# Performance work log

Measured on AMD Instinct MI355X. Metric: run time of the kernel, lower is better.

Reference implementation:

```python
import jax, jax.numpy as jnp
import numpy as np

BL = 5           # block_len
BS = BL * BL     # block_size = 25
NH = 8           # num_heads
MASK_ONES = 12   # first 12 window positions unmasked (causal raster mask)


def _rel_pos_index():
    coords = np.stack(np.meshgrid(np.arange(BL), np.arange(BL), indexing='ij')).reshape(2, -1)
    rel = coords[:, :, None] - coords[:, None, :]          # [2, 25, 25]
    idx = (rel[0] + BL - 1) * (2 * BL - 1) + (rel[1] + BL - 1)
    return idx                                              # [25, 25] int

_REL_IDX = _rel_pos_index()


def _layernorm(x, w, b, eps=1e-5):
    m = jnp.mean(x, axis=-1, keepdims=True)
    v = jnp.var(x, axis=-1, keepdims=True)
    return (x - m) * jax.lax.rsqrt(v + eps) * w + b


def setup_inputs() -> dict:
    key = jax.random.key(0)
    ks = jax.random.split(key, 16)
    B, C, H, W = 4, 64, 64, 64
    out_dim = 64
    hidden = int(C * 4.0)
    s = lambda k, shape, scale=0.02: jax.random.normal(k, shape, dtype=jnp.float32) * scale
    return {
        'x': jax.random.normal(ks[0], (B, C, H, W), dtype=jnp.float32),
        'norm1_w': jnp.ones((C,), jnp.float32), 'norm1_b': jnp.zeros((C,), jnp.float32),
        'qkv_w': s(ks[1], (3 * C, C)), 'qkv_b': s(ks[2], (3 * C,)),
        'rpb_table': s(ks[3], ((2 * BL - 1) * (2 * BL - 1), NH)),
        'norm2_w': jnp.ones((C,), jnp.float32), 'norm2_b': jnp.zeros((C,), jnp.float32),
        'fc1_w': s(ks[4], (hidden, C)), 'fc1_b': s(ks[5], (hidden,)),
        'fc2_w': s(ks[6], (C, hidden)), 'fc2_b': s(ks[7], (C,)),
        'proj_w': s(ks[8], (out_dim, C)), 'proj_b': s(ks[9], (out_dim,)),
    }


def reference(x, norm1_w, norm1_b, qkv_w, qkv_b, rpb_table,
              norm2_w, norm2_b, fc1_w, fc1_b, fc2_w, fc2_b, proj_w, proj_b):
    B, C, H, W = x.shape
    hd = C // NH
    scale = hd ** (-0.5)

    # F.unfold(kernel=5, pad=2): per-pixel 5x5 neighborhood, channel-major then (kh,kw)
    xp = jnp.pad(x, ((0, 0), (0, 0), (2, 2), (2, 2)))
    patches = jnp.stack([xp[:, :, i:i + H, j:j + W] for i in range(BL) for j in range(BL)], axis=2)  # [B,C,25,H,W]
    x_unfold = patches.reshape(B, C, BS, H * W).transpose(0, 3, 2, 1)  # [B,HW,25,C]

    mask = (jnp.arange(BS) < MASK_ONES).astype(x.dtype)[None, None, :, None]
    x_masked = x_unfold * mask

    out = _layernorm(x_masked, norm1_w, norm1_b)
    qkv = out @ qkv_w.T + qkv_b                                 # [B,HW,25,3C]
    qkv = qkv.reshape(B, H * W, BS, 3, NH, hd).transpose(3, 0, 1, 4, 2, 5)  # [3,B,HW,nh,25,hd]
    q, k, v = qkv[0] * scale, qkv[1], qkv[2]

    attn = jnp.einsum('bpnqd,bpnkd->bpnqk', q, k)               # [B,HW,nh,25,25]
    bias = rpb_table[_REL_IDX.reshape(-1)].reshape(BS, BS, NH).transpose(2, 0, 1)  # [nh,25,25]
    attn = jax.nn.softmax(attn + bias[None, None], axis=-1)

    o = jnp.einsum('bpnqk,bpnkd->bpnqd', attn, v)               # [B,HW,nh,25,hd]
    o = o.transpose(0, 1, 3, 2, 4).reshape(B, H * W, BS, C)
    o = o + x_masked
    out_sumed = jnp.sum(o, axis=2)                              # [B,HW,C]

    y = _layernorm(out_sumed, norm2_w, norm2_b)
    y = jax.nn.gelu(y @ fc1_w.T + fc1_b, approximate=False) @ fc2_w.T + fc2_b
    y = y + out_sumed
    y = y @ proj_w.T + proj_b                                   # [B,HW,out_dim]
    return y.reshape(B, H, W, -1).transpose(0, 3, 1, 2)
```

## Files before the change

### kernel.cpp

```cpp
#include <hip/hip_runtime.h>
#include <hip/hip_bf16.h>


typedef _Float16 h2f __attribute__((ext_vector_type(2)));
typedef _Float16 h8  __attribute__((ext_vector_type(8)));
union u8h { h8 v; h2f p[4]; };
union pk4 { _Float16 h[4]; unsigned int u[2]; };

__device__ __forceinline__ float fdot2f(h2f a, h2f b, float c) {
#if defined(__has_builtin)
#if __has_builtin(__builtin_amdgcn_fdot2)
    return __builtin_amdgcn_fdot2(a, b, c, false);
#else
    return c + (float)a.x*(float)b.x + (float)a.y*(float)b.y;
#endif
#else
    return c + (float)a.x*(float)b.x + (float)a.y*(float)b.y;
#endif
}
__device__ __forceinline__ float dot8(u8h a, u8h b) {
    float c = 0.f;
    c = fdot2f(a.p[0], b.p[0], c);
    c = fdot2f(a.p[1], b.p[1], c);
    c = fdot2f(a.p[2], b.p[2], c);
    c = fdot2f(a.p[3], b.p[3], c);
    return c;
}
__device__ __forceinline__ float frcp(float x) {
#if defined(__has_builtin)
#if __has_builtin(__builtin_amdgcn_rcpf)
    return __builtin_amdgcn_rcpf(x);
#else
    return 1.0f/x;
#endif
#else
    return 1.0f/x;
#endif
}
__device__ __forceinline__ u8h ldh8(const _Float16* p) { u8h r; __builtin_memcpy(&r, p, 16); return r; }
__device__ __forceinline__ void st16(_Float16* d, const float4& v) { __builtin_memcpy(d, &v, 16); }
__device__ __forceinline__ float4 ld16(const _Float16* p) { float4 v; __builtin_memcpy(&v, p, 16); return v; }

#define SC 0.35355339059327373f

__global__ __launch_bounds__(1024) void k_qkv(
    const float* __restrict__ x, const float* __restrict__ n1w, const float* __restrict__ n1b,
    const float* __restrict__ qw, const float* __restrict__ qb, const float* __restrict__ rpb,
    const float* __restrict__ w1, const float* __restrict__ w2, const float* __restrict__ pw,
    _Float16* __restrict__ qkvh, _Float16* __restrict__ qkvc_h, _Float16* __restrict__ eb7,
    _Float16* __restrict__ w1h, _Float16* __restrict__ w2h, _Float16* __restrict__ pwh,
    float* __restrict__ osT)
{
    __shared__ float smem[6208];
    const int t = threadIdx.x, bid = blockIdx.x;
    if (bid < 256) {
        _Float16* sOut = (_Float16*)smem;
        const int pix = t & 63, g = t >> 6;
        const int p = bid*64 + pix;
        const int b = p >> 12, hw = p & 4095;
        const float* xp = x + (size_t)b*262144 + hw;
        float xr[64]; float s = 0.f, s2 = 0.f;
        #pragma unroll
        for (int c = 0; c < 64; ++c) { float v = xp[(size_t)c*4096]; xr[c] = v; s += v; s2 += v*v; }
        float m = s*0.015625f;
        float rstd = rsqrtf(fmaxf(s2*0.015625f - m*m, 0.f) + 1e-5f);
        #pragma unroll
        for (int c = 0; c < 64; ++c) xr[c] = (xr[c] - m)*rstd*n1w[c] + n1b[c];
        #pragma unroll
        for (int i4 = 0; i4 < 12; i4 += 4) {
            const int o = g*12 + i4;
            const float* wr = qw + o*64;
            float a0 = qb[o], a1 = qb[o+1], a2 = qb[o+2], a3 = qb[o+3];
            #pragma unroll 16
            for (int c = 0; c < 64; ++c) {
                float xv = xr[c];
                a0 += xv*wr[c]; a1 += xv*wr[64+c]; a2 += xv*wr[128+c]; a3 += xv*wr[192+c];
            }
            pk4 pk;
            pk.h[0]=(_Float16)a0; pk.h[1]=(_Float16)a1; pk.h[2]=(_Float16)a2; pk.h[3]=(_Float16)a3;
            __builtin_memcpy(sOut + pix*194 + o, &pk, 8);
        }
        __syncthreads();
        for (int i = t; i < 1536; i += 1024) {
            int pp = i/24, d4 = i%24;
            ((float4*)qkvh)[(size_t)bid*1536 + i] = ld16(sOut + pp*194 + d4*8);
        }
        return;
    }
    if (bid < 512) {
        float* sxp = smem;
        const int plane = bid - 256;
        for (int i = t; i < 4624; i += 1024) sxp[i] = 0.f;
        __syncthreads();
        const float* xp = x + (size_t)plane*4096;
        for (int i = t; i < 4096; i += 1024) {
            int r = i >> 6, w = i & 63;
            sxp[(r + 2)*68 + (w + 2)] = xp[i];
        }
        __syncthreads();
        const int c = plane & 63, b = plane >> 6;
        float* op = osT + (size_t)c*16384 + b*4096;
        for (int i = t; i < 4096; i += 1024) {
            int r = i >> 6, w = i & 63;
            const float* s0 = sxp + r*68 + w;
            float sv = s0[0]+s0[1]+s0[2]+s0[3]+s0[4]
                     + s0[68]+s0[69]+s0[70]+s0[71]+s0[72]
                     + s0[136]+s0[137];
            op[i] = sv;
        }
        return;
    }
    if (bid < 520) {
        const int cid = bid - 512;
        for (int i = t; i < 4608; i += 1024) {
            int j = cid*4608 + i;
            if (j < 16384)      w1h[j]          = (_Float16)w1[j];
            else if (j < 32768) w2h[j - 16384]  = (_Float16)w2[j - 16384];
            else                pwh[j - 32768]  = (_Float16)pw[j - 32768];
        }
        return;
    }
    if (t < 192) {
        float acc = qb[t];
        for (int c = 0; c < 64; ++c) acc += n1b[c]*qw[t*64 + c];
        qkvc_h[t] = (_Float16)acc;
    }
    for (int i = t; i < 3200; i += 1024) {
        int j = i & 7, hf = (i >> 3) & 1, r = i >> 4;
        int h = r/25, q = r - h*25;
        float v = 0.f;
        if (j < 6) {
            int k = hf*6 + j;
            int ridx = (q/5 - k/5 + 4)*9 + (q%5 - k%5 + 4);
            v = __expf(rpb[ridx*8 + h]);
        } else if (j == 6 && hf) {
            for (int k = 12; k < 25; ++k) {
                int ridx = (q/5 - k/5 + 4)*9 + (q%5 - k%5 + 4);
                v += __expf(rpb[ridx*8 + h]);
            }
        }
        eb7[i] = (_Float16)v;
    }
}

__global__ __launch_bounds__(512) void k_attn(
    const _Float16* __restrict__ qkvh, const _Float16* __restrict__ qkvc_h,
    const _Float16* __restrict__ eb7g, float* __restrict__ osT)
{
    __shared__ _Float16 sq[108*194];
    __shared__ alignas(16) _Float16 seb[3200];
    __shared__ alignas(16) _Float16 sqc[192];
    const int t = threadIdx.x;
    const int p0 = blockIdx.x*32;
    const int b = p0 >> 12, hw0 = p0 & 4095, hrow = hw0 >> 6, w0c = hw0 & 63;

    for (int i = t; i < 1600; i += 512) ((unsigned int*)seb)[i] = ((const unsigned int*)eb7g)[i];
    if (t < 96) ((unsigned int*)sqc)[t] = ((const unsigned int*)qkvc_h)[t];
    for (int i = t; i < 2592; i += 512) {
        int row = i/24, d4 = i%24;
        int rr = row/36, cc = row%36;
        int gr = hrow - 2 + rr, gc = w0c - 2 + cc;
        float4 v = (gr >= 0 && gc >= 0 && gc < 64)
            ? ((const float4*)qkvh)[(size_t)((b << 12) + (gr << 6) + gc)*24 + d4]
            : ((const float4*)qkvc_h)[d4];
        st16(sq + row*194 + d4*8, v);
    }
    __syncthreads();

    const int pix = t & 31, hf = (t >> 5) & 1, h = t >> 6, hb = h*8;
    int rws[6];
    #pragma unroll
    for (int j = 0; j < 6; ++j) { int k = hf*6 + j; rws[j] = (k/5)*36 + pix + (k%5); }
    u8h kreg[7];
    #pragma unroll
    for (int j = 0; j < 6; ++j) kreg[j] = ldh8(sq + rws[j]*194 + 64 + hb);
    kreg[6] = hf ? ldh8(sqc + 64 + hb) : kreg[0];
    u8h qcu = ldh8(sqc + hb);
    float edc[7];
    #pragma unroll
    for (int j = 0; j < 7; ++j) edc[j] = __expf(dot8(qcu, kreg[j])*SC);
    float w[7];
    #pragma unroll
    for (int j = 0; j < 7; ++j) w[j] = 0.f;
    const _Float16* ebbase = seb + h*400 + hf*8;

    for (int sIdx = 0; sIdx < 12; ++sIdx) {
        int rq = (sIdx/5)*36 + pix + (sIdx%5);
        u8h qu = ldh8(sq + rq*194 + hb);
        h8 eb8; __builtin_memcpy(&eb8, ebbase + sIdx*16, 16);
        float e[7]; float rs = 0.f;
        #pragma unroll
        for (int j = 0; j < 7; ++j) {
            float ev = __expf(dot8(qu, kreg[j])*SC)*(float)eb8[j];
            e[j] = ev; rs += ev;
        }
        rs += __shfl_xor(rs, 32);
        float inv = frcp(rs);
        #pragma unroll
        for (int j = 0; j < 7; ++j) w[j] += e[j]*inv;
    }
    for (int q = 12; q < 25; ++q) {
        h8 eb8; __builtin_memcpy(&eb8, ebbase + q*16, 16);
        float e[7]; float rs = 0.f;
        #pragma unroll
        for (int j = 0; j < 7; ++j) {
            float ev = edc[j]*(float)eb8[j];
            e[j] = ev; rs += ev;
        }
        rs += __shfl_xor(rs, 32);
        float inv = frcp(rs);
        #pragma unroll
        for (int j = 0; j < 7; ++j) w[j] += e[j]*inv;
    }
    float out[8];
    #pragma unroll
    for (int d = 0; d < 8; ++d) out[d] = 0.f;
    #pragma unroll
    for (int j = 0; j < 7; ++j) {
        const _Float16* vp = (j < 6) ? (sq + rws[j]*194 + 128 + hb)
                                     : (hf ? sqc + 128 + hb : sq + rws[0]*194 + 128 + hb);
        u8h vv = ldh8(vp);
        float wj = w[j];
        #pragma unroll
        for (int d4 = 0; d4 < 4; ++d4) {
            h2f pr = vv.p[d4];
            out[d4*2]   += wj*(float)pr.x;
            out[d4*2+1] += wj*(float)pr.y;
        }
    }
    #pragma unroll
    for (int d = 0; d < 8; ++d) out[d] += __shfl_xor(out[d], 32);
    const int p = p0 + pix, dbase = hf*4;
    float* op = osT + (size_t)(hb + dbase)*16384 + p;
    op[0]     += out[dbase];
    op[16384] += out[dbase + 1];
    op[32768] += out[dbase + 2];
    op[49152] += out[dbase + 3];
}

__global__ __launch_bounds__(512) void k_mlp(
    const float* __restrict__ osT, const float* __restrict__ n2w, const float* __restrict__ n2b,
    const float* __restrict__ b1, const float* __restrict__ b2, const float* __restrict__ pb,
    const _Float16* __restrict__ w1h, const _Float16* __restrict__ w2h, const _Float16* __restrict__ pwh,
    float* __restrict__ out)
{
    __shared__ float sRed[2][576];
    __shared__ h2f  sAv[64*33];
    __shared__ alignas(16) _Float16 sH[64*258];
    __shared__ alignas(16) _Float16 sY[64*74];
    const int t = threadIdx.x;
    const int pix = t & 63, g = t >> 6;
    const int p = blockIdx.x*64 + pix;
    const int c0 = g*8;
    float v[8]; float ps = 0.f, ps2 = 0.f;
    #pragma unroll
    for (int j = 0; j < 8; ++j) {
        float vv = osT[(size_t)(c0 + j)*16384 + p];
        v[j] = vv; ps += vv; ps2 += vv*vv;
    }
    sRed[0][pix*9 + g] = ps;
    sRed[1][pix*9 + g] = ps2;
    __syncthreads();
    float s = 0.f, s2 = 0.f;
    #pragma unroll
    for (int gg = 0; gg < 8; ++gg) { s += sRed[0][pix*9 + gg]; s2 += sRed[1][pix*9 + gg]; }
    float m = s*0.015625f;
    float rstd = rsqrtf(fmaxf(s2*0.015625f - m*m, 0.f) + 1e-5f);
    #pragma unroll
    for (int k = 0; k < 4; ++k) {
        float e0 = (v[2*k]   - m)*rstd*n2w[c0 + 2*k]   + n2b[c0 + 2*k];
        float e1 = (v[2*k+1] - m)*rstd*n2w[c0 + 2*k+1] + n2b[c0 + 2*k+1];
        sAv[pix*33 + g*4 + k] = h2f{(_Float16)e0, (_Float16)e1};
    }
    __syncthreads();
    const h2f* avr = sAv + pix*33;
    #pragma unroll
    for (int i4 = 0; i4 < 32; i4 += 4) {
        const int j = g*32 + i4;
        const h2f* wr = (const h2f*)(w1h + (size_t)j*64);
        float a0 = b1[j], a1 = b1[j+1], a2 = b1[j+2], a3 = b1[j+3];
        #pragma unroll
        for (int cp = 0; cp < 32; ++cp) {
            h2f xv = avr[cp];
            a0 = fdot2f(xv, wr[cp],      a0);
            a1 = fdot2f(xv, wr[32 + cp], a1);
            a2 = fdot2f(xv, wr[64 + cp], a2);
            a3 = fdot2f(xv, wr[96 + cp], a3);
        }
        sH[pix*258 + j]     = (_Float16)(0.5f*a0*(1.f + erff(a0*0.70710678f)));
        sH[pix*258 + j + 1] = (_Float16)(0.5f*a1*(1.f + erff(a1*0.70710678f)));
        sH[pix*258 + j + 2] = (_Float16)(0.5f*a2*(1.f + erff(a2*0.70710678f)));
        sH[pix*258 + j + 3] = (_Float16)(0.5f*a3*(1.f + erff(a3*0.70710678f)));
    }
    __syncthreads();
    const h2f* hr = (const h2f*)(sH + pix*258);
    #pragma unroll
    for (int m4 = 0; m4 < 8; m4 += 4) {
        const int o = g*8 + m4;
        const h2f* wr = (const h2f*)(w2h + (size_t)o*256);
        float a0 = b2[o], a1 = b2[o+1], a2 = b2[o+2], a3 = b2[o+3];
        #pragma unroll 32
        for (int jp = 0; jp < 128; ++jp) {
            h2f hv = hr[jp];
            a0 = fdot2f(hv, wr[jp],       a0);
            a1 = fdot2f(hv, wr[128 + jp], a1);
            a2 = fdot2f(hv, wr[256 + jp], a2);
            a3 = fdot2f(hv, wr[384 + jp], a3);
        }
        a0 += osT[(size_t)o*16384 + p];
        a1 += osT[(size_t)(o+1)*16384 + p];
        a2 += osT[(size_t)(o+2)*16384 + p];
        a3 += osT[(size_t)(o+3)*16384 + p];
        sY[pix*74 + o]     = (_Float16)a0;
        sY[pix*74 + o + 1] = (_Float16)a1;
        sY[pix*74 + o + 2] = (_Float16)a2;
        sY[pix*74 + o + 3] = (_Float16)a3;
    }
    __syncthreads();
    const h2f* yr = (const h2f*)(sY + pix*74);
    const int bimg = p >> 12, hw = p & 4095, hh = hw >> 6;
    #pragma unroll
    for (int m4 = 0; m4 < 8; m4 += 4) {
        const int o = g*8 + m4;
        const h2f* wr = (const h2f*)(pwh + (size_t)o*64);
        float a0 = pb[o], a1 = pb[o+1], a2 = pb[o+2], a3 = pb[o+3];
        #pragma unroll
        for (int cp = 0; cp < 32; ++cp) {
            h2f yv = yr[cp];
            a0 = fdot2f(yv, wr[cp],      a0);
            a1 = fdot2f(yv, wr[32 + cp], a1);
            a2 = fdot2f(yv, wr[64 + cp], a2);
            a3 = fdot2f(yv, wr[96 + cp], a3);
        }
        float* ob = out + ((size_t)((bimg*64 + o)*64 + hh))*64 + pix;
        ob[0]     = a0;
        ob[4096]  = a1;
        ob[8192]  = a2;
        ob[12288] = a3;
    }
}

extern "C" void kernel_launch(void* const* d_in, const int* in_sizes, int n_in,
                              void* d_out, int out_size, void* d_ws, size_t ws_size,
                              hipStream_t stream) {
    const float* x   = (const float*)d_in[0];
    const float* n1w = (const float*)d_in[1];
    const float* n1b = (const float*)d_in[2];
    const float* qw  = (const float*)d_in[3];
    const float* qb  = (const float*)d_in[4];
    const float* rpb = (const float*)d_in[5];
    const float* n2w = (const float*)d_in[6];
    const float* n2b = (const float*)d_in[7];
    const float* w1  = (const float*)d_in[8];
    const float* b1  = (const float*)d_in[9];
    const float* w2  = (const float*)d_in[10];
    const float* b2  = (const float*)d_in[11];
    const float* pw  = (const float*)d_in[12];
    const float* pb  = (const float*)d_in[13];
    float* out = (float*)d_out;

    float* ws = (float*)d_ws;
    _Float16* qkvh   = (_Float16*)ws;
    float*    osT    = ws + 1572864;
    _Float16* qkvc_h = (_Float16*)(ws + 2621440);
    _Float16* eb7    = (_Float16*)(ws + 2621536);
    _Float16* w1h    = (_Float16*)(ws + 2623136);
    _Float16* w2h    = (_Float16*)(ws + 2631328);
    _Float16* pwh    = (_Float16*)(ws + 2639520);

    hipLaunchKernelGGL(k_qkv, dim3(521), dim3(1024), 0, stream,
                       x, n1w, n1b, qw, qb, rpb, w1, w2, pw,
                       qkvh, qkvc_h, eb7, w1h, w2h, pwh, osT);
    hipLaunchKernelGGL(k_attn, dim3(512), dim3(512), 0, stream,
                       qkvh, qkvc_h, eb7, osT);
    hipLaunchKernelGGL(k_mlp, dim3(256), dim3(512), 0, stream,
                       osT, n2w, n2b, b1, b2, pb, w1h, w2h, pwh, out);
}
```

Baseline: 217.8 us.

## Fuse attention and MLP kernels; stage x through shared memory in QKV

Merges the attention kernel and the MLP/projection kernel into one launch. Each 32-pixel block keeps its attention output plus residual in shared memory and runs layernorm, fc1, GELU, fc2 and proj from there, so the osT read-modify-write and the second global read of osT go away. Shared memory regions are aliased across phases. The QKV kernel now loads its x tile cooperatively into padded shared memory before the per-pixel layernorm. The trade-offs are extra barriers, larger shared memory per block (possibly lower occupancy) and smaller MLP blocks that reload weights more often.

```diff
diff --git a/kernel.cpp b/kernel.cpp
--- a/kernel.cpp
+++ b/kernel.cpp
@@ -51,17 +51,22 @@
     _Float16* __restrict__ w1h, _Float16* __restrict__ w2h, _Float16* __restrict__ pwh,
     float* __restrict__ osT)
 {
-    __shared__ float smem[6208];
+    __shared__ float smem[10368];
     const int t = threadIdx.x, bid = blockIdx.x;
     if (bid < 256) {
-        _Float16* sOut = (_Float16*)smem;
+        float* sXf = smem;
+        _Float16* sOut = (_Float16*)(smem + 4160);
+        const int p0 = bid*64;
+        const int b = p0 >> 12, hw0 = p0 & 4095;
+        for (int i = t; i < 4096; i += 1024) {
+            int c = i >> 6, pp = i & 63;
+            sXf[pp*65 + c] = x[(size_t)b*262144 + (size_t)c*4096 + hw0 + pp];
+        }
+        __syncthreads();
         const int pix = t & 63, g = t >> 6;
-        const int p = bid*64 + pix;
-        const int b = p >> 12, hw = p & 4095;
-        const float* xp = x + (size_t)b*262144 + hw;
         float xr[64]; float s = 0.f, s2 = 0.f;
         #pragma unroll
-        for (int c = 0; c < 64; ++c) { float v = xp[(size_t)c*4096]; xr[c] = v; s += v; s2 += v*v; }
+        for (int c = 0; c < 64; ++c) { float v = sXf[pix*65 + c]; xr[c] = v; s += v; s2 += v*v; }
         float m = s*0.015625f;
         float rstd = rsqrtf(fmaxf(s2*0.015625f - m*m, 0.f) + 1e-5f);
         #pragma unroll
@@ -143,13 +148,25 @@
     }
 }
 
-__global__ __launch_bounds__(512) void k_attn(
+__global__ __launch_bounds__(512) void k_fused(
     const _Float16* __restrict__ qkvh, const _Float16* __restrict__ qkvc_h,
-    const _Float16* __restrict__ eb7g, float* __restrict__ osT)
+    const _Float16* __restrict__ eb7g, const float* __restrict__ osT,
+    const float* __restrict__ n2w, const float* __restrict__ n2b,
+    const float* __restrict__ b1, const float* __restrict__ b2, const float* __restrict__ pb,
+    const _Float16* __restrict__ w1h, const _Float16* __restrict__ w2h, const _Float16* __restrict__ pwh,
+    float* __restrict__ out)
 {
-    __shared__ _Float16 sq[108*194];
-    __shared__ alignas(16) _Float16 seb[3200];
-    __shared__ alignas(16) _Float16 sqc[192];
+    __shared__ alignas(16) char smem[57040];
+    _Float16* sq   = (_Float16*)(smem);
+    _Float16* seb  = (_Float16*)(smem + 41920);
+    _Float16* sqc  = (_Float16*)(smem + 48320);
+    float*    sOs  = (float*)   (smem + 48704);
+    _Float16* sH   = (_Float16*)(smem);
+    h2f*      sAv  = (h2f*)     (smem + 16512);
+    float*    sRW  = (float*)   (smem + 20880);
+    float*    sMR  = (float*)   (smem + 23008);
+    _Float16* sY   = (_Float16*)(smem + 41920);
+
     const int t = threadIdx.x;
     const int p0 = blockIdx.x*32;
     const int b = p0 >> 12, hw0 = p0 & 4095, hrow = hw0 >> 6, w0c = hw0 & 63;
@@ -165,139 +182,147 @@
             : ((const float4*)qkvc_h)[d4];
         st16(sq + row*194 + d4*8, v);
     }
-    __syncthreads();
-
-    const int pix = t & 31, hf = (t >> 5) & 1, h = t >> 6, hb = h*8;
-    int rws[6];
+    for (int i = t; i < 2048; i += 512) {
+        int c = i >> 5, pp = i & 31;
+        sOs[pp*65 + c] = osT[(size_t)c*16384 + p0 + pp];
+    }
+    __syncthreads();
+
+    {
+        const int pix = t & 31, hf = (t >> 5) & 1, h = t >> 6, hb = h*8;
+        int rws[6];
+        #pragma unroll
+        for (int j = 0; j < 6; ++j) { int k = hf*6 + j; rws[j] = (k/5)*36 + pix + (k%5); }
+        u8h kreg[7];
+        #pragma unroll
+        for (int j = 0; j < 6; ++j) kreg[j] = ldh8(sq + rws[j]*194 + 64 + hb);
+        kreg[6] = hf ? ldh8(sqc + 64 + hb) : kreg[0];
+        u8h qcu = ldh8(sqc + hb);
+        float edc[7];
+        #pragma unroll
+        for (int j = 0; j < 7; ++j) edc[j] = __expf(dot8(qcu, kreg[j])*SC);
+        float w[7];
+        #pragma unroll
+        for (int j = 0; j < 7; ++j) w[j] = 0.f;
+        const _Float16* ebbase = seb + h*400 + hf*8;
+
+        for (int sIdx = 0; sIdx < 12; ++sIdx) {
+            int rq = (sIdx/5)*36 + pix + (sIdx%5);
+            u8h qu = ldh8(sq + rq*194 + hb);
+            h8 eb8; __builtin_memcpy(&eb8, ebbase + sIdx*16, 16);
+            float e[7]; float rs = 0.f;
+            #pragma unroll
+            for (int j = 0; j < 7; ++j) {
+                float ev = __expf(dot8(qu, kreg[j])*SC)*(float)eb8[j];
+                e[j] = ev; rs += ev;
+            }
+            rs += __shfl_xor(rs, 32);
+            float inv = frcp(rs);
+            #pragma unroll
+            for (int j = 0; j < 7; ++j) w[j] += e[j]*inv;
+        }
+        for (int q = 12; q < 25; ++q) {
+            h8 eb8; __builtin_memcpy(&eb8, ebbase + q*16, 16);
+            float e[7]; float rs = 0.f;
+            #pragma unroll
+            for (int j = 0; j < 7; ++j) {
+                float ev = edc[j]*(float)eb8[j];
+                e[j] = ev; rs += ev;
+            }
+            rs += __shfl_xor(rs, 32);
+            float inv = frcp(rs);
+            #pragma unroll
+            for (int j = 0; j < 7; ++j) w[j] += e[j]*inv;
+        }
+        float o8[8];
+        #pragma unroll
+        for (int d = 0; d < 8; ++d) o8[d] = 0.f;
+        #pragma unroll
+        for (int j = 0; j < 7; ++j) {
+            const _Float16* vp = (j < 6) ? (sq + rws[j]*194 + 128 + hb)
+                                         : (hf ? sqc + 128 + hb : sq + rws[0]*194 + 128 + hb);
+            u8h vv = ldh8(vp);
+            float wj = w[j];
+            #pragma unroll
+            for (int d4 = 0; d4 < 4; ++d4) {
+                h2f pr = vv.p[d4];
+                o8[d4*2]   += wj*(float)pr.x;
+                o8[d4*2+1] += wj*(float)pr.y;
+            }
+        }
+        #pragma unroll
+        for (int d = 0; d < 8; ++d) o8[d] += __shfl_xor(o8[d], 32);
+        const int c0 = hb + hf*4;
+        float* ap = sOs + pix*65 + c0;
+        #pragma unroll
+        for (int j = 0; j < 4; ++j) ap[j] += o8[hf*4 + j];
+    }
+    __syncthreads();
+
+    const int pix = t & 31, sl = t >> 5;
+    const int c4 = sl*4;
+    float ps = 0.f, ps2 = 0.f;
+    float vch[4];
     #pragma unroll
-    for (int j = 0; j < 6; ++j) { int k = hf*6 + j; rws[j] = (k/5)*36 + pix + (k%5); }
-    u8h kreg[7];
-    #pragma unroll
-    for (int j = 0; j < 6; ++j) kreg[j] = ldh8(sq + rws[j]*194 + 64 + hb);
-    kreg[6] = hf ? ldh8(sqc + 64 + hb) : kreg[0];
-    u8h qcu = ldh8(sqc + hb);
-    float edc[7];
-    #pragma unroll
-    for (int j = 0; j < 7; ++j) edc[j] = __expf(dot8(qcu, kreg[j])*SC);
-    float w[7];
-    #pragma unroll
-    for (int j = 0; j < 7; ++j) w[j] = 0.f;
-    const _Float16* ebbase = seb + h*400 + hf*8;
-
-    for (int sIdx = 0; sIdx < 12; ++sIdx) {
-        int rq = (sIdx/5)*36 + pix + (sIdx%5);
-        u8h qu = ldh8(sq + rq*194 + hb);
-        h8 eb8; __builtin_memcpy(&eb8, ebbase + sIdx*16, 16);
-        float e[7]; float rs = 0.f;
-        #pragma unroll
-        for (int j = 0; j < 7; ++j) {
-            float ev = __expf(dot8(qu, kreg[j])*SC)*(float)eb8[j];
-            e[j] = ev; rs += ev;
-        }
-        rs += __shfl_xor(rs, 32);
-        float inv = frcp(rs);
-        #pragma unroll
-        for (int j = 0; j < 7; ++j) w[j] += e[j]*inv;
-    }
-    for (int q = 12; q < 25; ++q) {
-        h8 eb8; __builtin_memcpy(&eb8, ebbase + q*16, 16);
-        float e[7]; float rs = 0.f;
-        #pragma unroll
-        for (int j = 0; j < 7; ++j) {
-            float ev = edc[j]*(float)eb8[j];
-            e[j] = ev; rs += ev;
-        }
-        rs += __shfl_xor(rs, 32);
-        float inv = frcp(rs);
-        #pragma unroll
-        for (int j = 0; j < 7; ++j) w[j] += e[j]*inv;
-    }
-    float out[8];
-    #pragma unroll
-    for (int d = 0; d < 8; ++d) out[d] = 0.f;
-    #pragma unroll
-    for (int j = 0; j < 7; ++j) {
-        const _Float16* vp = (j < 6) ? (sq + rws[j]*194 + 128 + hb)
-                                     : (hf ? sqc + 128 + hb : sq + rws[0]*194 + 128 + hb);
-        u8h vv = ldh8(vp);
-        float wj = w[j];
-        #pragma unroll
-        for (int d4 = 0; d4 < 4; ++d4) {
-            h2f pr = vv.p[d4];
-            out[d4*2]   += wj*(float)pr.x;
-            out[d4*2+1] += wj*(float)pr.y;
-        }
-    }
-    #pragma unroll
-    for (int d = 0; d < 8; ++d) out[d] += __shfl_xor(out[d], 32);
-    const int p = p0 + pix, dbase = hf*4;
-    float* op = osT + (size_t)(hb + dbase)*16384 + p;
-    op[0]     += out[dbase];
-    op[16384] += out[dbase + 1];
-    op[32768] += out[dbase + 2];
-    op[49152] += out[dbase + 3];
-}
-
-__global__ __launch_bounds__(512) void k_mlp(
-    const float* __restrict__ osT, const float* __restrict__ n2w, const float* __restrict__ n2b,
-    const float* __restrict__ b1, const float* __restrict__ b2, const float* __restrict__ pb,
-    const _Float16* __restrict__ w1h, const _Float16* __restrict__ w2h, const _Float16* __restrict__ pwh,
-    float* __restrict__ out)
-{
-    __shared__ float sRed[2][576];
-    __shared__ h2f  sAv[64*33];
-    __shared__ alignas(16) _Float16 sH[64*258];
-    __shared__ alignas(16) _Float16 sY[64*74];
-    const int t = threadIdx.x;
-    const int pix = t & 63, g = t >> 6;
-    const int p = blockIdx.x*64 + pix;
-    const int c0 = g*8;
-    float v[8]; float ps = 0.f, ps2 = 0.f;
-    #pragma unroll
-    for (int j = 0; j < 8; ++j) {
-        float vv = osT[(size_t)(c0 + j)*16384 + p];
-        v[j] = vv; ps += vv; ps2 += vv*vv;
-    }
-    sRed[0][pix*9 + g] = ps;
-    sRed[1][pix*9 + g] = ps2;
-    __syncthreads();
-    float s = 0.f, s2 = 0.f;
-    #pragma unroll
-    for (int gg = 0; gg < 8; ++gg) { s += sRed[0][pix*9 + gg]; s2 += sRed[1][pix*9 + gg]; }
-    float m = s*0.015625f;
-    float rstd = rsqrtf(fmaxf(s2*0.015625f - m*m, 0.f) + 1e-5f);
-    #pragma unroll
-    for (int k = 0; k < 4; ++k) {
-        float e0 = (v[2*k]   - m)*rstd*n2w[c0 + 2*k]   + n2b[c0 + 2*k];
-        float e1 = (v[2*k+1] - m)*rstd*n2w[c0 + 2*k+1] + n2b[c0 + 2*k+1];
-        sAv[pix*33 + g*4 + k] = h2f{(_Float16)e0, (_Float16)e1};
-    }
-    __syncthreads();
-    const h2f* avr = sAv + pix*33;
-    #pragma unroll
-    for (int i4 = 0; i4 < 32; i4 += 4) {
-        const int j = g*32 + i4;
-        const h2f* wr = (const h2f*)(w1h + (size_t)j*64);
-        float a0 = b1[j], a1 = b1[j+1], a2 = b1[j+2], a3 = b1[j+3];
-        #pragma unroll
-        for (int cp = 0; cp < 32; ++cp) {
-            h2f xv = avr[cp];
-            a0 = fdot2f(xv, wr[cp],      a0);
-            a1 = fdot2f(xv, wr[32 + cp], a1);
-            a2 = fdot2f(xv, wr[64 + cp], a2);
-            a3 = fdot2f(xv, wr[96 + cp], a3);
-        }
-        sH[pix*258 + j]     = (_Float16)(0.5f*a0*(1.f + erff(a0*0.70710678f)));
-        sH[pix*258 + j + 1] = (_Float16)(0.5f*a1*(1.f + erff(a1*0.70710678f)));
-        sH[pix*258 + j + 2] = (_Float16)(0.5f*a2*(1.f + erff(a2*0.70710678f)));
-        sH[pix*258 + j + 3] = (_Float16)(0.5f*a3*(1.f + erff(a3*0.70710678f)));
-    }
-    __syncthreads();
-    const h2f* hr = (const h2f*)(sH + pix*258);
-    #pragma unroll
-    for (int m4 = 0; m4 < 8; m4 += 4) {
-        const int o = g*8 + m4;
+    for (int j = 0; j < 4; ++j) {
+        float v = sOs[pix*65 + c4 + j];
+        vch[j] = v; ps += v; ps2 += v*v;
+    }
+    ps  += __shfl_xor(ps, 32);
+    ps2 += __shfl_xor(ps2, 32);
+    const int wv = t >> 6;
+    if (((t >> 5) & 1) == 0) {
+        sRW[(wv*33 + pix)*2]     = ps;
+        sRW[(wv*33 + pix)*2 + 1] = ps2;
+    }
+    __syncthreads();
+    if (t < 32) {
+        float s = 0.f, s2 = 0.f;
+        #pragma unroll
+        for (int g = 0; g < 8; ++g) { s += sRW[(g*33 + t)*2]; s2 += sRW[(g*33 + t)*2 + 1]; }
+        float m = s*0.015625f;
+        sMR[t*2]     = m;
+        sMR[t*2 + 1] = rsqrtf(fmaxf(s2*0.015625f - m*m, 0.f) + 1e-5f);
+    }
+    __syncthreads();
+    {
+        float m = sMR[pix*2], r = sMR[pix*2 + 1];
+        #pragma unroll
+        for (int j = 0; j < 2; ++j) {
+            float e0 = (vch[2*j]   - m)*r*n2w[c4 + 2*j]   + n2b[c4 + 2*j];
+            float e1 = (vch[2*j+1] - m)*r*n2w[c4 + 2*j+1] + n2b[c4 + 2*j+1];
+            sAv[pix*34 + sl*2 + j] = h2f{(_Float16)e0, (_Float16)e1};
+        }
+    }
+    __syncthreads();
+
+    {
+        const h2f* avr = sAv + pix*34;
+        #pragma unroll
+        for (int i4 = 0; i4 < 16; i4 += 4) {
+            const int j = sl*16 + i4;
+            const h2f* wr = (const h2f*)(w1h + (size_t)j*64);
+            float a0 = b1[j], a1 = b1[j+1], a2 = b1[j+2], a3 = b1[j+3];
+            #pragma unroll
+            for (int cp = 0; cp < 32; ++cp) {
+                h2f xv = avr[cp];
+                a0 = fdot2f(xv, wr[cp],      a0);
+                a1 = fdot2f(xv, wr[32 + cp], a1);
+                a2 = fdot2f(xv, wr[64 + cp], a2);
+                a3 = fdot2f(xv, wr[96 + cp], a3);
+            }
+            sH[pix*258 + j]     = (_Float16)(0.5f*a0*(1.f + erff(a0*0.70710678f)));
+            sH[pix*258 + j + 1] = (_Float16)(0.5f*a1*(1.f + erff(a1*0.70710678f)));
+            sH[pix*258 + j + 2] = (_Float16)(0.5f*a2*(1.f + erff(a2*0.70710678f)));
+            sH[pix*258 + j + 3] = (_Float16)(0.5f*a3*(1.f + erff(a3*0.70710678f)));
+        }
+    }
+    __syncthreads();
+
+    {
+        const int o = sl*4;
         const h2f* wr = (const h2f*)(w2h + (size_t)o*256);
+        const h2f* hr = (const h2f*)(sH + pix*258);
         float a0 = b2[o], a1 = b2[o+1], a2 = b2[o+2], a3 = b2[o+3];
         #pragma unroll 32
         for (int jp = 0; jp < 128; ++jp) {
@@ -307,22 +332,21 @@
             a2 = fdot2f(hv, wr[256 + jp], a2);
             a3 = fdot2f(hv, wr[384 + jp], a3);
         }
-        a0 += osT[(size_t)o*16384 + p];
-        a1 += osT[(size_t)(o+1)*16384 + p];
-        a2 += osT[(size_t)(o+2)*16384 + p];
-        a3 += osT[(size_t)(o+3)*16384 + p];
+        a0 += sOs[pix*65 + o];
+        a1 += sOs[pix*65 + o + 1];
+        a2 += sOs[pix*65 + o + 2];
+        a3 += sOs[pix*65 + o + 3];
         sY[pix*74 + o]     = (_Float16)a0;
         sY[pix*74 + o + 1] = (_Float16)a1;
         sY[pix*74 + o + 2] = (_Float16)a2;
         sY[pix*74 + o + 3] = (_Float16)a3;
     }
     __syncthreads();
-    const h2f* yr = (const h2f*)(sY + pix*74);
-    const int bimg = p >> 12, hw = p & 4095, hh = hw >> 6;
-    #pragma unroll
-    for (int m4 = 0; m4 < 8; m4 += 4) {
-        const int o = g*8 + m4;
+
+    {
+        const int o = sl*4;
         const h2f* wr = (const h2f*)(pwh + (size_t)o*64);
+        const h2f* yr = (const h2f*)(sY + pix*74);
         float a0 = pb[o], a1 = pb[o+1], a2 = pb[o+2], a3 = pb[o+3];
         #pragma unroll
         for (int cp = 0; cp < 32; ++cp) {
@@ -332,7 +356,9 @@
             a2 = fdot2f(yv, wr[64 + cp], a2);
             a3 = fdot2f(yv, wr[96 + cp], a3);
         }
-        float* ob = out + ((size_t)((bimg*64 + o)*64 + hh))*64 + pix;
+        const int p = p0 + pix;
+        const int bimg = p >> 12, hw = p & 4095, hh = hw >> 6, ww = hw & 63;
+        float* ob = out + ((size_t)((bimg*64 + o)*64 + hh))*64 + ww;
         ob[0]     = a0;
         ob[4096]  = a1;
         ob[8192]  = a2;
@@ -371,8 +397,7 @@
     hipLaunchKernelGGL(k_qkv, dim3(521), dim3(1024), 0, stream,
                        x, n1w, n1b, qw, qb, rpb, w1, w2, pw,
                        qkvh, qkvc_h, eb7, w1h, w2h, pwh, osT);
-    hipLaunchKernelGGL(k_attn, dim3(512), dim3(512), 0, stream,
-                       qkvh, qkvc_h, eb7, osT);
-    hipLaunchKernelGGL(k_mlp, dim3(256), dim3(512), 0, stream,
-                       osT, n2w, n2b, b1, b2, pb, w1h, w2h, pwh, out);
-}
+    hipLaunchKernelGGL(k_fused, dim3(512), dim3(512), 0, stream,
+                       qkvh, qkvc_h, eb7, osT,
+                       n2w, n2b, b1, b2, pb, w1h, w2h, pwh, out);
+}
```

New measurement: 215.0 us. No clear change (-1.3%).
